# Optimization experiments

Hardware: AMD Instinct MI355X
Metric: run time of the kernel (lower is better)

The kernel has to match this reference:

```python
import jax, jax.numpy as jnp
import numpy as np

DMODEL = 512
NUM_HEADS = 8
DK = DMODEL // NUM_HEADS  # 64
CAUSAL = True


def setup_inputs() -> dict:
    key = jax.random.key(0)
    ks = jax.random.split(key, 11)
    B, S = 4, 2048
    s_in = 1.0 / np.sqrt(DMODEL)
    s_out = 1.0 / np.sqrt(NUM_HEADS * DK)
    return {
        "Q": jax.random.normal(ks[0], (B, S, DMODEL), jnp.float32),
        "K": jax.random.normal(ks[1], (B, S, DMODEL), jnp.float32),
        "V": jax.random.normal(ks[2], (B, S, DMODEL), jnp.float32),
        # torch nn.Linear weights stored as [in, out] (already transposed)
        "WQ_w": jax.random.uniform(ks[3], (DMODEL, DK), jnp.float32, -s_in, s_in),
        "WQ_b": jax.random.uniform(ks[4], (DK,), jnp.float32, -s_in, s_in),
        "WK_w": jax.random.uniform(ks[5], (DMODEL, DK), jnp.float32, -s_in, s_in),
        "WK_b": jax.random.uniform(ks[6], (DK,), jnp.float32, -s_in, s_in),
        "WV_w": jax.random.uniform(ks[7], (DMODEL, DK), jnp.float32, -s_in, s_in),
        "WV_b": jax.random.uniform(ks[8], (DK,), jnp.float32, -s_in, s_in),
        "Wo_w": jax.random.uniform(ks[9], (NUM_HEADS * DK, DMODEL), jnp.float32, -s_out, s_out),
        "Wo_b": jax.random.uniform(ks[10], (DMODEL,), jnp.float32, -s_out, s_out),
    }


def reference(Q, K, V, WQ_w, WQ_b, WK_w, WK_b, WV_w, WV_b, Wo_w, Wo_b):
    # Single shared projection to dk=64 (NOT per-head in the original module)
    q = Q @ WQ_w + WQ_b  # [B,S,dk]
    k = K @ WK_w + WK_b  # [B,S,dk]
    v = V @ WV_w + WV_b  # [B,S,dk]
    scores = jnp.einsum("bsd,btd->bst", q, k) / np.sqrt(DK).astype(np.float32)
    if CAUSAL:
        S = scores.shape[-1]
        causal = jnp.tril(jnp.ones((S, S), dtype=bool))  # True = keep
        scores = jnp.where(causal, scores, -jnp.inf)
    attn = jax.nn.softmax(scores, axis=-1)
    head_out = jnp.einsum("bst,btd->bsd", attn, v)  # [B,S,dk]
    # Every head is identical -> concat == tile num_heads copies
    concat = jnp.tile(head_out, (1, 1, NUM_HEADS))  # [B,S,num_heads*dk]
    return concat @ Wo_w + Wo_b  # [B,S,dmodel]
```

## Files before the change

kernel.cpp:

```cpp
#include <hip/hip_runtime.h>
#include <hip/hip_bf16.h>

#define DMODEL 512
#define DK 64
#define NH 8
#define SEQ 2048
#define BATCH 4
#define NROWS 8192
#define NEGBIG -1.0e30f
#define SPLITW 8
#define DKP 66
#define SHIFT 6.0f

typedef _Float16 half_t;
typedef _Float16 half8 __attribute__((ext_vector_type(8)));
typedef _Float16 half4 __attribute__((ext_vector_type(4)));
typedef float floatx4 __attribute__((ext_vector_type(4)));

#if defined(__has_builtin)
#if __has_builtin(__builtin_amdgcn_mfma_f32_16x16x16f16)
#define HAVE_MFMA16X16X16 1
#else
#define HAVE_MFMA16X16X16 0
#endif
#else
#define HAVE_MFMA16X16X16 0
#endif

__global__ __launch_bounds__(256) void prep_kernel(
    const float* __restrict__ WQ, const float* __restrict__ WK,
    const float* __restrict__ WV, const float* __restrict__ Wo,
    half_t* __restrict__ wtq, half_t* __restrict__ wtk, half_t* __restrict__ wtv,
    half_t* __restrict__ wo_tr)
{
    const int idx = blockIdx.x * 256 + threadIdx.x;
    const int n = idx >> 9;
    const int k = idx & 511;
    wtq[idx] = (half_t)WQ[k * DK + n];
    wtk[idx] = (half_t)WK[k * DK + n];
    wtv[idx] = (half_t)WV[k * DK + n];
    const int n2 = idx >> 6;
    const int k2 = idx & 63;
    float s = 0.f;
#pragma unroll
    for (int h = 0; h < NH; h++)
        s += Wo[((size_t)(h * DK + k2)) * DMODEL + n2];
    wo_tr[idx] = (half_t)s;
}

__global__ __launch_bounds__(128) void proj_kernel(
    const float* __restrict__ Q, const float* __restrict__ K, const float* __restrict__ V,
    const half_t* __restrict__ wtq, const half_t* __restrict__ wtk, const half_t* __restrict__ wtv,
    const float* __restrict__ bQ, const float* __restrict__ bK, const float* __restrict__ bV,
    half_t* __restrict__ qh, half_t* __restrict__ kh, half_t* __restrict__ vt)
{
    const int tens = blockIdx.y;
    const float* X  = (tens == 0) ? Q : (tens == 1) ? K : V;
    const half_t* wt = (tens == 0) ? wtq : (tens == 1) ? wtk : wtv;
    const float* bias = (tens == 0) ? bQ : (tens == 1) ? bK : bV;

    const int r0 = blockIdx.x * 16;
    const int tid = threadIdx.x;
    const int w = tid >> 6;
    const int lane = tid & 63;
    const int c = lane & 15;
    const int quad = lane >> 4;

    __shared__ floatx4 red[4][64];

    floatx4 acc[4] = {{0.f,0.f,0.f,0.f},{0.f,0.f,0.f,0.f},{0.f,0.f,0.f,0.f},{0.f,0.f,0.f,0.f}};

    const float* xrow = X + (size_t)(r0 + c) * DMODEL + quad * 8;
#pragma unroll 8
    for (int ks = w; ks < 16; ks += 2) {
        const float* xp = xrow + ks * 32;
        half8 a;
#pragma unroll
        for (int i = 0; i < 8; i++) a[i] = (half_t)xp[i];
#pragma unroll
        for (int nt = 0; nt < 4; nt++) {
            half8 bfr = *(const half8*)(wt + (size_t)(nt * 16 + c) * DMODEL + ks * 32 + quad * 8);
            acc[nt] = __builtin_amdgcn_mfma_f32_16x16x32_f16(a, bfr, acc[nt], 0, 0, 0);
        }
    }

    if (w == 1) {
#pragma unroll
        for (int nt = 0; nt < 4; nt++) red[nt][lane] = acc[nt];
    }
    __syncthreads();
    if (w == 1) return;

#pragma unroll
    for (int nt = 0; nt < 4; nt++) {
        const floatx4 r4 = red[nt][lane];
        const float bv = bias[nt * 16 + c];
#pragma unroll
        for (int r = 0; r < 4; r++) {
            const float val = acc[nt][r] + r4[r] + bv;
            const int row = r0 + quad * 4 + r;
            if (tens == 0) {
                qh[(size_t)row * DK + nt * 16 + c] = (half_t)val;
            } else if (tens == 1) {
                kh[(size_t)row * DK + nt * 16 + c] = (half_t)val;
            } else {
                const int b  = row >> 11;
                const int s  = row & (SEQ - 1);
                const int kb = s >> 4;
                const int kk = s & 15;
                vt[((((size_t)b * 128 + kb) * 4 + nt) * 16 + c) * 16 + kk] = (half_t)val;
            }
        }
    }
}

__global__ __launch_bounds__(512, 4) void attn_kernel(
    const half_t* __restrict__ qh, const half_t* __restrict__ kh,
    const half_t* __restrict__ vt, const half_t* __restrict__ wo_tr,
    const float* __restrict__ bo, float* __restrict__ out)
{
    const int bx = blockIdx.x;
    int b, qt;
    if (bx < 256) { qt = bx >> 1;            b = bx & 1; }
    else          { int k2 = bx - 256; qt = 127 - (k2 >> 1); b = 2 + (k2 & 1); }
    const int tid = threadIdx.x;
    const int w = tid >> 6;
    const int lane = tid & 63;
    const int c = lane & 15;
    const int quad = lane >> 4;

    __shared__ float sow[SPLITW][16][DKP];
    __shared__ float sl_s[SPLITW][16];
    __shared__ half_t of16[16][72];

    const half_t* qrow = qh + (size_t)(b * SEQ + qt * 16 + c) * DK + quad * 8;
    half8 qb0 = *(const half8*)(qrow);
    half8 qb1 = *(const half8*)(qrow + 32);
#pragma unroll
    for (int i = 0; i < 8; i++) { qb0[i] = qb0[i] * (half_t)0.125f; qb1[i] = qb1[i] * (half_t)0.125f; }

    float lp = 0.f;
    floatx4 o[4] = {{0.f,0.f,0.f,0.f},{0.f,0.f,0.f,0.f},{0.f,0.f,0.f,0.f},{0.f,0.f,0.f,0.f}};
    const floatx4 cinit = {-SHIFT, -SHIFT, -SHIFT, -SHIFT};

    const half_t* kbb = kh + (size_t)b * SEQ * DK;
    const half_t* vtb = vt + (size_t)b * 128 * 1024;

    int pb = w;
    half8 ka0, ka1, kb0, kb1;
    if (2 * pb <= qt) {
        const half_t* kr0 = kbb + (size_t)(2 * pb * 16 + c) * DK + quad * 8;
        ka0 = *(const half8*)(kr0);
        ka1 = *(const half8*)(kr0 + 32);
        const half_t* kr1 = kr0 + 16 * DK;
        kb0 = *(const half8*)(kr1);
        kb1 = *(const half8*)(kr1 + 32);
    }

    while (2 * pb <= qt) {
        const int t0 = 2 * pb, t1 = 2 * pb + 1;
        const half_t* vk0 = vtb + (size_t)t0 * 1024;
        const half_t* vk1 = vtb + (size_t)t1 * 1024;
#if HAVE_MFMA16X16X16
        half4 va0 = *(const half4*)(vk0 + ((size_t)0 * 16 + c) * 16 + quad * 4);
        half4 va1 = *(const half4*)(vk0 + ((size_t)1 * 16 + c) * 16 + quad * 4);
        half4 va2 = *(const half4*)(vk0 + ((size_t)2 * 16 + c) * 16 + quad * 4);
        half4 va3 = *(const half4*)(vk0 + ((size_t)3 * 16 + c) * 16 + quad * 4);
        half4 vc0 = *(const half4*)(vk1 + ((size_t)0 * 16 + c) * 16 + quad * 4);
        half4 vc1 = *(const half4*)(vk1 + ((size_t)1 * 16 + c) * 16 + quad * 4);
        half4 vc2 = *(const half4*)(vk1 + ((size_t)2 * 16 + c) * 16 + quad * 4);
        half4 vc3 = *(const half4*)(vk1 + ((size_t)3 * 16 + c) * 16 + quad * 4);
#else
        half8 va80 = *(const half8*)(vk0 + ((size_t)0 * 16 + c) * 16 + (quad & 1) * 8);
        half8 va81 = *(const half8*)(vk0 + ((size_t)1 * 16 + c) * 16 + (quad & 1) * 8);
        half8 va82 = *(const half8*)(vk0 + ((size_t)2 * 16 + c) * 16 + (quad & 1) * 8);
        half8 va83 = *(const half8*)(vk0 + ((size_t)3 * 16 + c) * 16 + (quad & 1) * 8);
        half8 vc80 = *(const half8*)(vk1 + ((size_t)0 * 16 + c) * 16 + (quad & 1) * 8);
        half8 vc81 = *(const half8*)(vk1 + ((size_t)1 * 16 + c) * 16 + (quad & 1) * 8);
        half8 vc82 = *(const half8*)(vk1 + ((size_t)2 * 16 + c) * 16 + (quad & 1) * 8);
        half8 vc83 = *(const half8*)(vk1 + ((size_t)3 * 16 + c) * 16 + (quad & 1) * 8);
#endif
        const int npb = pb + SPLITW;
        half8 nka0 = ka0, nka1 = ka1, nkb0 = kb0, nkb1 = kb1;
        if (2 * npb <= qt) {
            const half_t* nkr0 = kbb + (size_t)(2 * npb * 16 + c) * DK + quad * 8;
            nka0 = *(const half8*)(nkr0);
            nka1 = *(const half8*)(nkr0 + 32);
            const half_t* nkr1 = nkr0 + 16 * DK;
            nkb0 = *(const half8*)(nkr1);
            nkb1 = *(const half8*)(nkr1 + 32);
        }

        floatx4 sc0 = cinit;
        sc0 = __builtin_amdgcn_mfma_f32_16x16x32_f16(ka0, qb0, sc0, 0, 0, 0);
        sc0 = __builtin_amdgcn_mfma_f32_16x16x32_f16(ka1, qb1, sc0, 0, 0, 0);
        floatx4 sc1 = cinit;
        sc1 = __builtin_amdgcn_mfma_f32_16x16x32_f16(kb0, qb0, sc1, 0, 0, 0);
        sc1 = __builtin_amdgcn_mfma_f32_16x16x32_f16(kb1, qb1, sc1, 0, 0, 0);

        if (t0 == qt) {
#pragma unroll
            for (int r = 0; r < 4; r++) {
                if (quad * 4 + r > c) sc0[r] = NEGBIG;
                sc1[r] = NEGBIG;
            }
        } else if (t1 == qt) {
#pragma unroll
            for (int r = 0; r < 4; r++)
                if (quad * 4 + r > c) sc1[r] = NEGBIG;
        }

        float p0[4], p1[4];
#pragma unroll
        for (int r = 0; r < 4; r++) { p0[r] = __expf(sc0[r]); p1[r] = __expf(sc1[r]); }
        lp += (p0[0] + p0[1] + p0[2] + p0[3]) + (p1[0] + p1[1] + p1[2] + p1[3]);

#if HAVE_MFMA16X16X16
        half4 pa, pc;
#pragma unroll
        for (int r = 0; r < 4; r++) { pa[r] = (half_t)p0[r]; pc[r] = (half_t)p1[r]; }
        o[0] = __builtin_amdgcn_mfma_f32_16x16x16f16(pa, va0, o[0], 0, 0, 0);
        o[1] = __builtin_amdgcn_mfma_f32_16x16x16f16(pa, va1, o[1], 0, 0, 0);
        o[2] = __builtin_amdgcn_mfma_f32_16x16x16f16(pa, va2, o[2], 0, 0, 0);
        o[3] = __builtin_amdgcn_mfma_f32_16x16x16f16(pa, va3, o[3], 0, 0, 0);
        o[0] = __builtin_amdgcn_mfma_f32_16x16x16f16(pc, vc0, o[0], 0, 0, 0);
        o[1] = __builtin_amdgcn_mfma_f32_16x16x16f16(pc, vc1, o[1], 0, 0, 0);
        o[2] = __builtin_amdgcn_mfma_f32_16x16x16f16(pc, vc2, o[2], 0, 0, 0);
        o[3] = __builtin_amdgcn_mfma_f32_16x16x16f16(pc, vc3, o[3], 0, 0, 0);
#else
        half8 pa8, pc8;
#pragma unroll
        for (int j = 0; j < 8; j++) {
            const int src = (((quad * 2 + (j >> 2)) & 3) * 16 + c);
            const float pj0 = __shfl(p0[j & 3], src);
            const float pj1 = __shfl(p1[j & 3], src);
            pa8[j] = (quad < 2) ? (half_t)pj0 : (half_t)0.f;
            pc8[j] = (quad < 2) ? (half_t)pj1 : (half_t)0.f;
        }
        o[0] = __builtin_amdgcn_mfma_f32_16x16x32_f16(pa8, va80, o[0], 0, 0, 0);
        o[1] = __builtin_amdgcn_mfma_f32_16x16x32_f16(pa8, va81, o[1], 0, 0, 0);
        o[2] = __builtin_amdgcn_mfma_f32_16x16x32_f16(pa8, va82, o[2], 0, 0, 0);
        o[3] = __builtin_amdgcn_mfma_f32_16x16x32_f16(pa8, va83, o[3], 0, 0, 0);
        o[0] = __builtin_amdgcn_mfma_f32_16x16x32_f16(pc8, vc80, o[0], 0, 0, 0);
        o[1] = __builtin_amdgcn_mfma_f32_16x16x32_f16(pc8, vc81, o[1], 0, 0, 0);
        o[2] = __builtin_amdgcn_mfma_f32_16x16x32_f16(pc8, vc82, o[2], 0, 0, 0);
        o[3] = __builtin_amdgcn_mfma_f32_16x16x32_f16(pc8, vc83, o[3], 0, 0, 0);
#endif
        ka0 = nka0; ka1 = nka1; kb0 = nkb0; kb1 = nkb1; pb = npb;
    }

    lp += __shfl_xor(lp, 16);
    lp += __shfl_xor(lp, 32);

#pragma unroll
    for (int nt = 0; nt < 4; nt++)
#pragma unroll
        for (int r = 0; r < 4; r++)
            sow[w][quad * 4 + r][nt * 16 + c] = o[nt][r];
    if (quad == 0) sl_s[w][c] = lp;
    __syncthreads();

    {
        const int q = w * 2 + (lane >> 5);
        const int d0 = (lane & 31) * 2;
        float lstar = 0.f, acc0 = 0.f, acc1 = 0.f;
#pragma unroll
        for (int ww = 0; ww < SPLITW; ww++) {
            lstar += sl_s[ww][q];
            const float* sp = &sow[ww][q][d0];
            acc0 += sp[0];
            acc1 += sp[1];
        }
        const float linv = 1.f / lstar;
        of16[q][d0]     = (half_t)(acc0 * linv);
        of16[q][d0 + 1] = (half_t)(acc1 * linv);
    }
    __syncthreads();

    half8 a1 = *(const half8*)(&of16[c][quad * 8]);
    half8 a2 = *(const half8*)(&of16[c][32 + quad * 8]);
    const size_t orow = (size_t)(b * SEQ + qt * 16);
#pragma unroll
    for (int i = 0; i < 4; i++) {
        const int n = (w * 4 + i) * 16 + c;
        half8 b1 = *(const half8*)(wo_tr + (size_t)n * DK + quad * 8);
        half8 b2 = *(const half8*)(wo_tr + (size_t)n * DK + 32 + quad * 8);
        floatx4 oc = {0.f, 0.f, 0.f, 0.f};
        oc = __builtin_amdgcn_mfma_f32_16x16x32_f16(a1, b1, oc, 0, 0, 0);
        oc = __builtin_amdgcn_mfma_f32_16x16x32_f16(a2, b2, oc, 0, 0, 0);
        const float bv = bo[n];
#pragma unroll
        for (int r = 0; r < 4; r++)
            out[(orow + quad * 4 + r) * DMODEL + n] = oc[r] + bv;
    }
}

extern "C" void kernel_launch(void* const* d_in, const int* in_sizes, int n_in,
                              void* d_out, int out_size, void* d_ws, size_t ws_size,
                              hipStream_t stream) {
    const float* Q  = (const float*)d_in[0];
    const float* K  = (const float*)d_in[1];
    const float* V  = (const float*)d_in[2];
    const float* WQ = (const float*)d_in[3];
    const float* bQ = (const float*)d_in[4];
    const float* WK = (const float*)d_in[5];
    const float* bK = (const float*)d_in[6];
    const float* WV = (const float*)d_in[7];
    const float* bV = (const float*)d_in[8];
    const float* Wo = (const float*)d_in[9];
    const float* bo = (const float*)d_in[10];
    float* out = (float*)d_out;

    char* ws = (char*)d_ws;
    half_t* qh    = (half_t*)ws;
    half_t* kh    = (half_t*)(ws + (1u << 20));
    half_t* vt    = (half_t*)(ws + (2u << 20));
    half_t* wtq   = (half_t*)(ws + (3u << 20));
    half_t* wtk   = wtq + 32768;
    half_t* wtv   = wtk + 32768;
    half_t* wo_tr = wtv + 32768;

    prep_kernel<<<128, 256, 0, stream>>>(WQ, WK, WV, Wo, wtq, wtk, wtv, wo_tr);
    proj_kernel<<<dim3(512, 3), 128, 0, stream>>>(Q, K, V, wtq, wtk, wtv, bQ, bK, bV, qh, kh, vt);
    attn_kernel<<<512, 512, 0, stream>>>(qh, kh, vt, wo_tr, bo, out);
}
```

Baseline: 140.4 us.

## Fuse prep, projection and attention into one cooperative kernel with grid syncs

Merges the three launches into a single cooperative kernel that runs weight prep, the QKV projection and attention in phases separated by grid-wide syncs. This removes two kernel launch gaps and their tail effects. The projection work is also regrouped so each wave computes a whole 16-row tile over the full K dimension, with no LDS reduction between two waves. If the cooperative launch fails, it falls back to three separate kernels. Grid syncs add overhead, and the launch depends on all 512 blocks being co-resident at 4 blocks per CU.

Result: slower. 271.3 us (+93.3%).

```diff
diff --git a/kernel.cpp b/kernel.cpp
--- a/kernel.cpp
+++ b/kernel.cpp
@@ -1,5 +1,8 @@
 #include <hip/hip_runtime.h>
 #include <hip/hip_bf16.h>
+#include <hip/hip_cooperative_groups.h>
+
+namespace cg = cooperative_groups;
 
 #define DMODEL 512
 #define DK 64
@@ -27,13 +30,13 @@
 #define HAVE_MFMA16X16X16 0
 #endif
 
-__global__ __launch_bounds__(256) void prep_kernel(
+
+__device__ __forceinline__ void prep_body(int idx,
     const float* __restrict__ WQ, const float* __restrict__ WK,
     const float* __restrict__ WV, const float* __restrict__ Wo,
     half_t* __restrict__ wtq, half_t* __restrict__ wtk, half_t* __restrict__ wtv,
     half_t* __restrict__ wo_tr)
 {
-    const int idx = blockIdx.x * 256 + threadIdx.x;
     const int n = idx >> 9;
     const int k = idx & 511;
     wtq[idx] = (half_t)WQ[k * DK + n];
@@ -48,31 +51,25 @@
     wo_tr[idx] = (half_t)s;
 }
 
-__global__ __launch_bounds__(128) void proj_kernel(
+__device__ __forceinline__ void proj_tile(int tens, int tile, int lane,
     const float* __restrict__ Q, const float* __restrict__ K, const float* __restrict__ V,
     const half_t* __restrict__ wtq, const half_t* __restrict__ wtk, const half_t* __restrict__ wtv,
     const float* __restrict__ bQ, const float* __restrict__ bK, const float* __restrict__ bV,
     half_t* __restrict__ qh, half_t* __restrict__ kh, half_t* __restrict__ vt)
 {
-    const int tens = blockIdx.y;
     const float* X  = (tens == 0) ? Q : (tens == 1) ? K : V;
     const half_t* wt = (tens == 0) ? wtq : (tens == 1) ? wtk : wtv;
     const float* bias = (tens == 0) ? bQ : (tens == 1) ? bK : bV;
 
-    const int r0 = blockIdx.x * 16;
-    const int tid = threadIdx.x;
-    const int w = tid >> 6;
-    const int lane = tid & 63;
+    const int r0 = tile * 16;
     const int c = lane & 15;
     const int quad = lane >> 4;
 
-    __shared__ floatx4 red[4][64];
-
     floatx4 acc[4] = {{0.f,0.f,0.f,0.f},{0.f,0.f,0.f,0.f},{0.f,0.f,0.f,0.f},{0.f,0.f,0.f,0.f}};
 
     const float* xrow = X + (size_t)(r0 + c) * DMODEL + quad * 8;
 #pragma unroll 8
-    for (int ks = w; ks < 16; ks += 2) {
+    for (int ks = 0; ks < 16; ks++) {
         const float* xp = xrow + ks * 32;
         half8 a;
 #pragma unroll
@@ -84,20 +81,12 @@
         }
     }
 
-    if (w == 1) {
-#pragma unroll
-        for (int nt = 0; nt < 4; nt++) red[nt][lane] = acc[nt];
-    }
-    __syncthreads();
-    if (w == 1) return;
-
 #pragma unroll
     for (int nt = 0; nt < 4; nt++) {
-        const floatx4 r4 = red[nt][lane];
         const float bv = bias[nt * 16 + c];
 #pragma unroll
         for (int r = 0; r < 4; r++) {
-            const float val = acc[nt][r] + r4[r] + bv;
+            const float val = acc[nt][r] + bv;
             const int row = r0 + quad * 4 + r;
             if (tens == 0) {
                 qh[(size_t)row * DK + nt * 16 + c] = (half_t)val;
@@ -114,24 +103,19 @@
     }
 }
 
-__global__ __launch_bounds__(512, 4) void attn_kernel(
+__device__ __forceinline__ void attn_body(int bx, int tid,
     const half_t* __restrict__ qh, const half_t* __restrict__ kh,
     const half_t* __restrict__ vt, const half_t* __restrict__ wo_tr,
-    const float* __restrict__ bo, float* __restrict__ out)
-{
-    const int bx = blockIdx.x;
+    const float* __restrict__ bo, float* __restrict__ out,
+    float (*sow)[16][DKP], float (*sl_s)[16], half_t (*of16)[72])
+{
     int b, qt;
     if (bx < 256) { qt = bx >> 1;            b = bx & 1; }
     else          { int k2 = bx - 256; qt = 127 - (k2 >> 1); b = 2 + (k2 & 1); }
-    const int tid = threadIdx.x;
     const int w = tid >> 6;
     const int lane = tid & 63;
     const int c = lane & 15;
     const int quad = lane >> 4;
-
-    __shared__ float sow[SPLITW][16][DKP];
-    __shared__ float sl_s[SPLITW][16];
-    __shared__ half_t of16[16][72];
 
     const half_t* qrow = qh + (size_t)(b * SEQ + qt * 16 + c) * DK + quad * 8;
     half8 qb0 = *(const half8*)(qrow);
@@ -295,6 +279,74 @@
     }
 }
 
+__global__ __launch_bounds__(512, 4) void fused_kernel(
+    const float* __restrict__ Q, const float* __restrict__ K, const float* __restrict__ V,
+    const float* __restrict__ WQ, const float* __restrict__ bQ,
+    const float* __restrict__ WK, const float* __restrict__ bK,
+    const float* __restrict__ WV, const float* __restrict__ bV,
+    const float* __restrict__ Wo, const float* __restrict__ bo,
+    half_t* __restrict__ qh, half_t* __restrict__ kh, half_t* __restrict__ vt,
+    half_t* __restrict__ wtq, half_t* __restrict__ wtk, half_t* __restrict__ wtv,
+    half_t* __restrict__ wo_tr, float* __restrict__ out)
+{
+    __shared__ float sow[SPLITW][16][DKP];
+    __shared__ float sl_s[SPLITW][16];
+    __shared__ half_t of16[16][72];
+
+    cg::grid_group grid = cg::this_grid();
+    const int tid = threadIdx.x;
+    const int bx = blockIdx.x;
+
+    {
+        const int gid = bx * 512 + tid;
+        if (gid < 32768)
+            prep_body(gid, WQ, WK, WV, Wo, wtq, wtk, wtv, wo_tr);
+    }
+    grid.sync();
+
+    {
+        const int g = bx * 8 + (tid >> 6);
+        if (g < 1536)
+            proj_tile(g >> 9, g & 511, tid & 63, Q, K, V, wtq, wtk, wtv,
+                      bQ, bK, bV, qh, kh, vt);
+    }
+    grid.sync();
+
+    attn_body(bx, tid, qh, kh, vt, wo_tr, bo, out, sow, sl_s, of16);
+}
+
+__global__ __launch_bounds__(256) void prep_kernel(
+    const float* __restrict__ WQ, const float* __restrict__ WK,
+    const float* __restrict__ WV, const float* __restrict__ Wo,
+    half_t* __restrict__ wtq, half_t* __restrict__ wtk, half_t* __restrict__ wtv,
+    half_t* __restrict__ wo_tr)
+{
+    prep_body(blockIdx.x * 256 + threadIdx.x, WQ, WK, WV, Wo, wtq, wtk, wtv, wo_tr);
+}
+
+__global__ __launch_bounds__(128) void proj_kernel(
+    const float* __restrict__ Q, const float* __restrict__ K, const float* __restrict__ V,
+    const half_t* __restrict__ wtq, const half_t* __restrict__ wtk, const half_t* __restrict__ wtv,
+    const float* __restrict__ bQ, const float* __restrict__ bK, const float* __restrict__ bV,
+    half_t* __restrict__ qh, half_t* __restrict__ kh, half_t* __restrict__ vt)
+{
+    const int g = blockIdx.x * 2 + (threadIdx.x >> 6);
+    if (g < 1536)
+        proj_tile(g >> 9, g & 511, threadIdx.x & 63, Q, K, V, wtq, wtk, wtv,
+                  bQ, bK, bV, qh, kh, vt);
+}
+
+__global__ __launch_bounds__(512, 4) void attn_kernel(
+    const half_t* __restrict__ qh, const half_t* __restrict__ kh,
+    const half_t* __restrict__ vt, const half_t* __restrict__ wo_tr,
+    const float* __restrict__ bo, float* __restrict__ out)
+{
+    __shared__ float sow[SPLITW][16][DKP];
+    __shared__ float sl_s[SPLITW][16];
+    __shared__ half_t of16[16][72];
+    attn_body(blockIdx.x, threadIdx.x, qh, kh, vt, wo_tr, bo, out, sow, sl_s, of16);
+}
+
 extern "C" void kernel_launch(void* const* d_in, const int* in_sizes, int n_in,
                               void* d_out, int out_size, void* d_ws, size_t ws_size,
                               hipStream_t stream) {
@@ -320,7 +372,19 @@
     half_t* wtv   = wtk + 32768;
     half_t* wo_tr = wtv + 32768;
 
-    prep_kernel<<<128, 256, 0, stream>>>(WQ, WK, WV, Wo, wtq, wtk, wtv, wo_tr);
-    proj_kernel<<<dim3(512, 3), 128, 0, stream>>>(Q, K, V, wtq, wtk, wtv, bQ, bK, bV, qh, kh, vt);
-    attn_kernel<<<512, 512, 0, stream>>>(qh, kh, vt, wo_tr, bo, out);
-}
+    void* args[] = {
+        (void*)&Q, (void*)&K, (void*)&V,
+        (void*)&WQ, (void*)&bQ, (void*)&WK, (void*)&bK, (void*)&WV, (void*)&bV,
+        (void*)&Wo, (void*)&bo,
+        (void*)&qh, (void*)&kh, (void*)&vt,
+        (void*)&wtq, (void*)&wtk, (void*)&wtv, (void*)&wo_tr,
+        (void*)&out
+    };
+    hipError_t err = hipLaunchCooperativeKernel((const void*)fused_kernel,
+                                                dim3(512), dim3(512), args, 0, stream);
+    if (err != hipSuccess) {
+        prep_kernel<<<128, 256, 0, stream>>>(WQ, WK, WV, Wo, wtq, wtk, wtv, wo_tr);
+        proj_kernel<<<768, 128, 0, stream>>>(Q, K, V, wtq, wtk, wtv, bQ, bK, bV, qh, kh, vt);
+        attn_kernel<<<512, 512, 0, stream>>>(qh, kh, vt, wo_tr, bo, out);
+    }
+}
```
